# Performance work log

Measured on AMD Instinct MI355X. Metric: run time of the kernel, lower is better.

Reference implementation:

```python
import jax, jax.numpy as jnp
import numpy as np

SIGMA_DIS = 3.0   # from init_kwargs
KMAX = 16         # max kernel label value (labels in 0..KMAX, 0 = background)


def setup_inputs() -> dict:
    key = jax.random.key(0)
    k1, k2 = jax.random.split(key)
    pred = jax.random.normal(k1, (16, 4, 640, 640), dtype=jnp.float32)
    labels = jax.random.randint(k2, (16, 640, 640), 0, KMAX + 1, dtype=jnp.int32)
    return {"pred_similarities": pred, "kernel_mask_ndi_labels": labels}


def _loss(pred, labels):
    # pred: (B, C, H, W) float; labels: (B, H, W) int in [0, KMAX]
    B, C = pred.shape[0], pred.shape[1]
    p = pred.reshape(B, C, -1)            # (B, C, P)
    lab = labels.reshape(B, -1)           # (B, P)
    sq = jnp.sum(p * p, axis=1)           # (B, P) per-pixel squared norm over channels

    # Per-segment sum of squared pred values and cardinality (scatter-reduce).
    seg_ss = jax.vmap(lambda s, l: jax.ops.segment_sum(s, l, num_segments=KMAX + 1))(sq, lab)            # (B, K+1)
    card = jax.vmap(lambda l: jax.ops.segment_sum(jnp.ones(l.shape, jnp.float32), l, num_segments=KMAX + 1))(lab)  # (B, K+1)

    # Masks for labels i and j are disjoint, so
    # ||pred*m_i/c_i - pred*m_j/c_j||_F^2 = SS_i/c_i^2 + SS_j/c_j^2 exactly.
    m = jnp.where(card > 0, seg_ss / jnp.square(jnp.maximum(card, 1.0)), 0.0)  # (B, K+1)

    ids = jnp.arange(KMAX + 1)
    pair_ok = (ids[:, None] >= 1) & (ids[None, :] > ids[:, None])               # i>=1, j>i
    valid = pair_ok[None, :, :] & (card[:, :, None] > 0) & (card[:, None, :] > 0)  # (B, K+1, K+1)

    s2 = m[:, :, None] + m[:, None, :]
    d = jnp.sqrt(jnp.where(valid, s2, 1.0))        # safe sqrt for masked-out pairs
    # NB: torch.max(norm, 0)[0] on a 0-dim tensor is the identity (no relu clamp) -> replicate.
    term = jnp.log1p(jnp.square(SIGMA_DIS - d))
    pair_sum = jnp.sum(jnp.where(valid, term, 0.0), axis=(1, 2))  # (B,)

    nk = jnp.max(lab, axis=1)                                      # num_kernels per image
    denom = (nk * (nk - 1)).astype(jnp.float32)
    loss_b = jnp.where(nk > 1, pair_sum / jnp.maximum(denom, 1.0), 0.0)
    return jnp.sum(loss_b)


def reference(pred_similarities, kernel_mask_ndi_labels):
    return _loss(pred_similarities, kernel_mask_ndi_labels)
```

## Files before the change

### kernel.cpp

```cpp
#include <hip/hip_runtime.h>

#define K   16
#define NB  16
#define NP  409600
#define NPV (NP / 4)
#define BX  128
#define NBLK (NB * BX)
#define SIGMA_DIS 3.0f

__global__ __launch_bounds__(256, 8) void seg_reduce_kernel(
    const float* __restrict__ pred,
    const int*   __restrict__ lab,
    float* __restrict__ ss_part,
    float* __restrict__ cnt_part)
{
    const int tid  = threadIdx.x;
    const int lane = tid & 63;
    const int wave = tid >> 6;
    const int b    = blockIdx.y;
    const int bx   = blockIdx.x;
    const int blk  = b * BX + bx;

    float ssb[K];
    int   cnt[K];
#pragma unroll
    for (int k = 0; k < K; ++k) { ssb[k] = 0.0f; cnt[k] = 0; }

    const float4* p0 = (const float4*)(pred + ((size_t)b * 4 + 0) * NP);
    const float4* p1 = (const float4*)(pred + ((size_t)b * 4 + 1) * NP);
    const float4* p2 = (const float4*)(pred + ((size_t)b * 4 + 2) * NP);
    const float4* p3 = (const float4*)(pred + ((size_t)b * 4 + 3) * NP);
    const int4*   lb = (const int4*)(lab + (size_t)b * NP);

    for (int v = bx * 256 + tid; v < NPV; v += BX * 256) {
        float4 a = p0[v];
        float4 c = p1[v];
        float4 d = p2[v];
        float4 e = p3[v];
        int4   l = lb[v];

        float s0 = a.x * a.x + c.x * c.x + d.x * d.x + e.x * e.x;
        float s1 = a.y * a.y + c.y * c.y + d.y * d.y + e.y * e.y;
        float s2 = a.z * a.z + c.z * c.z + d.z * d.z + e.z * e.z;
        float s3 = a.w * a.w + c.w * c.w + d.w * d.w + e.w * e.w;

#pragma unroll
        for (int k = 0; k < K; ++k) {
            const int kk = k + 1;
            bool e0 = (l.x == kk);
            bool e1 = (l.y == kk);
            bool e2 = (l.z == kk);
            bool e3 = (l.w == kk);
            ssb[k] += e0 ? s0 : 0.0f;
            ssb[k] += e1 ? s1 : 0.0f;
            ssb[k] += e2 ? s2 : 0.0f;
            ssb[k] += e3 ? s3 : 0.0f;
            cnt[k] += __popcll(__ballot(e0)) + __popcll(__ballot(e1))
                    + __popcll(__ballot(e2)) + __popcll(__ballot(e3));
        }
    }

#pragma unroll
    for (int k = 0; k < K; ++k) {
#pragma unroll
        for (int m = 1; m < 64; m <<= 1)
            ssb[k] += __shfl_xor(ssb[k], m, 64);
    }

    __shared__ float ss_sh[4][K];
    __shared__ int   cnt_sh[4][K];
    if (lane == 0) {
#pragma unroll
        for (int k = 0; k < K; ++k) { ss_sh[wave][k] = ssb[k]; cnt_sh[wave][k] = cnt[k]; }
    }
    __syncthreads();

    if (tid < K) {
        float s = ss_sh[0][tid] + ss_sh[1][tid] + ss_sh[2][tid] + ss_sh[3][tid];
        float c = (float)(cnt_sh[0][tid] + cnt_sh[1][tid] + cnt_sh[2][tid] + cnt_sh[3][tid]);
        ss_part [tid * NBLK + blk] = s;
        cnt_part[tid * NBLK + blk] = c;
    }
}

__global__ __launch_bounds__(256) void finalize_kernel(
    const float* __restrict__ ss_part,
    const float* __restrict__ cnt_part,
    float* __restrict__ out)
{
    __shared__ float m_sh[NB][K];
    __shared__ float c_sh[NB][K];
    __shared__ float inv_denom[NB];
    __shared__ float red[256];

    const int t = threadIdx.x;

    {
        const int fb = t >> 4;
        const int fk = t & 15;
        const float4* sp = (const float4*)(ss_part  + fk * NBLK + fb * BX);
        const float4* cp = (const float4*)(cnt_part + fk * NBLK + fb * BX);
        float ss = 0.0f, cc = 0.0f;
#pragma unroll
        for (int i = 0; i < BX / 4; ++i) {
            float4 v = sp[i];
            float4 w = cp[i];
            ss += v.x + v.y + v.z + v.w;
            cc += w.x + w.y + w.z + w.w;
        }
        c_sh[fb][fk] = cc;
        m_sh[fb][fk] = (cc > 0.0f) ? ss / (cc * cc) : 0.0f;
    }
    __syncthreads();

    if (t < NB) {
        int nk = 0;
        for (int k = K; k >= 1; --k) {
            if (c_sh[t][k - 1] > 0.0f) { nk = k; break; }
        }
        float denom = (float)(nk * (nk - 1));
        inv_denom[t] = (nk > 1) ? 1.0f / fmaxf(denom, 1.0f) : 0.0f;
    }
    __syncthreads();

    float acc = 0.0f;
    for (int e = t; e < NB * K * K; e += 256) {
        const int fb = e >> 8;
        const int ij = e & 255;
        const int ki = ij >> 4;
        const int kj = ij & 15;
        if (kj > ki && c_sh[fb][ki] > 0.0f && c_sh[fb][kj] > 0.0f) {
            float s2 = m_sh[fb][ki] + m_sh[fb][kj];
            float dd = sqrtf(s2);
            float x  = SIGMA_DIS - dd;
            acc += log1pf(x * x) * inv_denom[fb];
        }
    }

    red[t] = acc;
    __syncthreads();
    for (int s = 128; s > 0; s >>= 1) {
        if (t < s) red[t] += red[t + s];
        __syncthreads();
    }
    if (t == 0) out[0] = red[0];
}

extern "C" void kernel_launch(void* const* d_in, const int* in_sizes, int n_in,
                              void* d_out, int out_size, void* d_ws, size_t ws_size,
                              hipStream_t stream) {
    const float* pred = (const float*)d_in[0];
    const int*   lab  = (const int*)d_in[1];
    float* out = (float*)d_out;

    float* ss_part  = (float*)d_ws;
    float* cnt_part = ss_part + K * NBLK;

    dim3 grid(BX, NB);
    seg_reduce_kernel<<<grid, 256, 0, stream>>>(pred, lab, ss_part, cnt_part);
    finalize_kernel<<<1, 256, 0, stream>>>(ss_part, cnt_part, out);
}
```

Measured before the change: 46.89 us.

## Use contiguous per-block chunks, unroll loads, and replace ballot counts with per-thread counters

Halves the block count and gives each block a contiguous chunk, processed with two outstanding vector loads per iteration and a small tail. The per-label wave ballot and popcount is replaced by per-thread integer counters reduced by shuffles at the end. The aim is to cut ALU and scalar overhead in the inner loop and increase memory-level parallelism. The cost is more registers and fewer resident waves, since the occupancy hint is removed.

```diff
diff --git a/kernel.cpp b/kernel.cpp
--- a/kernel.cpp
+++ b/kernel.cpp
@@ -4,11 +4,12 @@
 #define NB  16
 #define NP  409600
 #define NPV (NP / 4)
-#define BX  128
+#define BX  64
+#define CHUNK (NPV / BX)
 #define NBLK (NB * BX)
 #define SIGMA_DIS 3.0f
 
-__global__ __launch_bounds__(256, 8) void seg_reduce_kernel(
+__global__ __launch_bounds__(256) void seg_reduce_kernel(
     const float* __restrict__ pred,
     const int*   __restrict__ lab,
     float* __restrict__ ss_part,
@@ -32,39 +33,60 @@
     const float4* p3 = (const float4*)(pred + ((size_t)b * 4 + 3) * NP);
     const int4*   lb = (const int4*)(lab + (size_t)b * NP);
 
-    for (int v = bx * 256 + tid; v < NPV; v += BX * 256) {
-        float4 a = p0[v];
-        float4 c = p1[v];
-        float4 d = p2[v];
-        float4 e = p3[v];
+    const int base = bx * CHUNK;
+
+#define ACCUM(LV, S0, S1, S2, S3)                                          \
+    _Pragma("unroll")                                                      \
+    for (int k = 0; k < K; ++k) {                                          \
+        const int kk = k + 1;                                              \
+        bool q0 = (LV.x == kk), q1 = (LV.y == kk);                         \
+        bool q2 = (LV.z == kk), q3 = (LV.w == kk);                         \
+        ssb[k] += (q0 ? S0 : 0.0f) + (q1 ? S1 : 0.0f)                      \
+                + (q2 ? S2 : 0.0f) + (q3 ? S3 : 0.0f);                     \
+        cnt[k] += (int)q0 + (int)q1 + (int)q2 + (int)q3;                   \
+    }
+
+#pragma unroll 1
+    for (int i = 0; i < 3; ++i) {
+        const int v0 = base + i * 512 + tid;
+        const int v1 = v0 + 256;
+
+        float4 a0 = p0[v0], c0 = p1[v0], d0 = p2[v0], e0 = p3[v0];
+        float4 a1 = p0[v1], c1 = p1[v1], d1 = p2[v1], e1 = p3[v1];
+        int4   l0 = lb[v0], l1 = lb[v1];
+
+        float s00 = a0.x*a0.x + c0.x*c0.x + d0.x*d0.x + e0.x*e0.x;
+        float s01 = a0.y*a0.y + c0.y*c0.y + d0.y*d0.y + e0.y*e0.y;
+        float s02 = a0.z*a0.z + c0.z*c0.z + d0.z*d0.z + e0.z*e0.z;
+        float s03 = a0.w*a0.w + c0.w*c0.w + d0.w*d0.w + e0.w*e0.w;
+        float s10 = a1.x*a1.x + c1.x*c1.x + d1.x*d1.x + e1.x*e1.x;
+        float s11 = a1.y*a1.y + c1.y*c1.y + d1.y*d1.y + e1.y*e1.y;
+        float s12 = a1.z*a1.z + c1.z*c1.z + d1.z*d1.z + e1.z*e1.z;
+        float s13 = a1.w*a1.w + c1.w*c1.w + d1.w*d1.w + e1.w*e1.w;
+
+        ACCUM(l0, s00, s01, s02, s03)
+        ACCUM(l1, s10, s11, s12, s13)
+    }
+
+    if (tid < CHUNK - 3 * 512) {
+        const int v = base + 3 * 512 + tid;
+        float4 a = p0[v], c = p1[v], d = p2[v], e = p3[v];
         int4   l = lb[v];
-
-        float s0 = a.x * a.x + c.x * c.x + d.x * d.x + e.x * e.x;
-        float s1 = a.y * a.y + c.y * c.y + d.y * d.y + e.y * e.y;
-        float s2 = a.z * a.z + c.z * c.z + d.z * d.z + e.z * e.z;
-        float s3 = a.w * a.w + c.w * c.w + d.w * d.w + e.w * e.w;
-
-#pragma unroll
-        for (int k = 0; k < K; ++k) {
-            const int kk = k + 1;
-            bool e0 = (l.x == kk);
-            bool e1 = (l.y == kk);
-            bool e2 = (l.z == kk);
-            bool e3 = (l.w == kk);
-            ssb[k] += e0 ? s0 : 0.0f;
-            ssb[k] += e1 ? s1 : 0.0f;
-            ssb[k] += e2 ? s2 : 0.0f;
-            ssb[k] += e3 ? s3 : 0.0f;
-            cnt[k] += __popcll(__ballot(e0)) + __popcll(__ballot(e1))
-                    + __popcll(__ballot(e2)) + __popcll(__ballot(e3));
-        }
+        float s0 = a.x*a.x + c.x*c.x + d.x*d.x + e.x*e.x;
+        float s1 = a.y*a.y + c.y*c.y + d.y*d.y + e.y*e.y;
+        float s2 = a.z*a.z + c.z*c.z + d.z*d.z + e.z*e.z;
+        float s3 = a.w*a.w + c.w*c.w + d.w*d.w + e.w*e.w;
+        ACCUM(l, s0, s1, s2, s3)
     }
+#undef ACCUM
 
 #pragma unroll
     for (int k = 0; k < K; ++k) {
 #pragma unroll
-        for (int m = 1; m < 64; m <<= 1)
+        for (int m = 1; m < 64; m <<= 1) {
             ssb[k] += __shfl_xor(ssb[k], m, 64);
+            cnt[k] += __shfl_xor(cnt[k], m, 64);
+        }
     }
 
     __shared__ float ss_sh[4][K];
```

Result: faster. 42.59 us (-9.2%).
